# Performance work log

Hardware: AMD Instinct MI355X
Metric: run time of the kernel (lower is better)

The kernel has to match this reference:

```python
import jax, jax.numpy as jnp
import numpy as np
import math

NLAT, NLON = 46, 90      # equiangular grid (in_shape == out_shape)
CH = 256                 # channels == kdim == vdim
BATCH = 1

def _cc_weights(n):
    # Clenshaw-Curtis quadrature weights (Waldvogel), nodes cos(k*pi/(n-1)); matches torch-harmonics equiangular grid
    n1 = n - 1
    N = np.arange(1, n1, 2)
    l = len(N)
    m = n1 - l
    v = np.concatenate([2.0 / N / (N - 2), [1.0 / N[-1]], np.zeros(m)])
    v = -v[:-1] - v[-1:0:-1]
    g0 = -np.ones(n1)
    g0[l] += n1
    g0[m] += n1
    g = g0 / (n1 ** 2 - 1 + (n1 % 2))
    w = np.fft.ifft(v + g).real
    return np.concatenate([w, w[:1]])

def _precompute_sparsity():
    # replicates _precompute_neighborhood_sparsity_s2: YZY-rotated north pole indicator within theta_cutoff
    lats = np.linspace(0.0, math.pi, NLAT)               # colatitudes of equiangular grid
    quad = (2.0 * math.pi / NLON) * _cc_weights(NLAT)    # per-latitude quadrature weights
    cutoff = math.pi / (NLAT - 1)                        # default theta_cutoff
    lons = np.linspace(0.0, 2.0 * math.pi, NLON + 1)[:-1]
    rows, cols = [], []
    for t in range(NLAT):
        a = -lats[t]
        beta = lons[None, :]
        gamma = lats[:, None]
        z = -np.cos(beta) * np.sin(a) * np.sin(gamma) + np.cos(a) * np.cos(gamma)
        x = np.cos(a) * np.cos(beta) * np.sin(gamma) + np.cos(gamma) * np.sin(a)
        y = np.sin(beta) * np.sin(gamma)
        nrm = np.sqrt(x * x + y * y + z * z)
        theta = np.arccos(np.clip(z / nrm, -1.0, 1.0))
        ii, jj = np.nonzero(theta <= cutoff)
        rows.append(np.full(ii.shape, t, dtype=np.int64))
        cols.append(ii * NLON + jj)
    row_ids = np.concatenate(rows).astype(np.int32)   # CSR row id per nnz (sorted)
    col_idx = np.concatenate(cols).astype(np.int32)   # flattened input index (at wo=0)
    return row_ids, col_idx, quad.astype(np.float32)

def setup_inputs() -> dict:
    key = jax.random.key(0)
    ks = jax.random.split(key, 9)
    row_ids, col_idx, quad = _precompute_sparsity()
    scale = 0.02  # sane init scale (module uses raw randn; trained weights would be O(this))
    return {
        "qo": jax.random.normal(ks[0], (BATCH, CH, NLAT, NLON), dtype=jnp.float32),
        "ki": jax.random.normal(ks[1], (BATCH, CH, NLAT, NLON), dtype=jnp.float32),
        "vi": jax.random.normal(ks[2], (BATCH, CH, NLAT, NLON), dtype=jnp.float32),
        "q_w": jax.random.normal(ks[3], (CH, CH), dtype=jnp.float32) * scale,
        "k_w": jax.random.normal(ks[4], (CH, CH), dtype=jnp.float32) * scale,
        "v_w": jax.random.normal(ks[5], (CH, CH), dtype=jnp.float32) * scale,
        "q_b": jax.random.normal(ks[6], (CH,), dtype=jnp.float32) * scale,
        "k_b": jax.random.normal(ks[7], (CH,), dtype=jnp.float32) * scale,
        "v_b": jax.random.normal(ks[8], (CH,), dtype=jnp.float32) * scale,
        "quad_w": jnp.asarray(quad),
        "row_ids": jnp.asarray(row_ids),
        "col_idx": jnp.asarray(col_idx),
    }

def reference(qo, ki, vi, q_w, k_w, v_w, q_b, k_b, v_b, quad_w, row_ids, col_idx):
    nlat, nlon = qo.shape[2], qo.shape[3]
    # 1x1 conv projections (F.conv2d with [out,in,1,1] kernels)
    q = jnp.einsum("kc,bchw->bkhw", q_w, qo) + q_b[None, :, None, None]
    k = jnp.einsum("kc,bchw->bkhw", k_w, ki) + k_b[None, :, None, None]
    v = jnp.einsum("vc,bchw->bvhw", v_w, vi) + v_b[None, :, None, None]

    hi = col_idx // nlon                                   # [N] input latitude per nnz
    wi0 = col_idx % nlon                                   # [N] input longitude at wo=0
    wo = jnp.arange(nlon)
    wi = (wi0[:, None] + wo[None, :]) % nlon               # [N, nlon] longitudes rotated by output lon

    kg = k[:, :, hi[:, None], wi]                          # [B, kdim, N, nlon] gathered keys
    qg = q[:, :, row_ids, :]                               # [B, kdim, N, nlon] query of owning output row
    qdotk = jnp.einsum("bcnw,bcnw->nbw", qg, kg)           # [N, B, nlon]

    # quadrature-weighted softmax over each output point's neighborhood (segment = output latitude row)
    seg_max = jax.ops.segment_max(qdotk, row_ids, num_segments=nlat, indices_are_sorted=True)
    seg_max = jax.lax.stop_gradient(seg_max)               # max shift cancels exactly in the ratio
    alpha = jnp.exp(qdotk - seg_max[row_ids]) * quad_w[hi][:, None, None]   # [N, B, nlon]
    denom = jax.ops.segment_sum(alpha, row_ids, num_segments=nlat, indices_are_sorted=True)  # [nlat, B, nlon]

    vg = jnp.transpose(v[:, :, hi[:, None], wi], (2, 0, 1, 3))   # [N, B, vdim, nlon]
    num = jax.ops.segment_sum(alpha[:, :, None, :] * vg, row_ids, num_segments=nlat, indices_are_sorted=True)
    out = num / denom[:, :, None, :]                       # [nlat, B, vdim, nlon]
    return jnp.transpose(out, (1, 2, 0, 3))                # [B, vdim, nlat, nlon]
```

## Files before the change

### kernel.cpp

```cpp
#include <hip/hip_runtime.h>
#include <math.h>

#define NLAT 46
#define NLON 90
#define CH   256
#define HW   (NLAT*NLON)
#define HWP  4160

#define LIGHT_PER_XCD 473
#define SLOTS_PER_XCD (45 + LIGHT_PER_XCD)

typedef __attribute__((ext_vector_type(8))) short short8;
typedef __attribute__((ext_vector_type(4))) float floatx4;

__device__ __forceinline__ ushort f2bf(float f){
  uint u = __float_as_uint(f);
  u += 0x7fff + ((u >> 16) & 1);
  return (ushort)(u >> 16);
}
__device__ __forceinline__ float bf2f(ushort u){
  return __uint_as_float(((uint)u) << 16);
}

__device__ __forceinline__ int lower_bound_i(const int* __restrict__ a, int n, int key){
  int lo = 0, hi = n;
  while (lo < hi){ int mid = (lo + hi) >> 1; if (a[mid] < key) lo = mid + 1; else hi = mid; }
  return lo;
}

__global__ __launch_bounds__(256) void cast_w_kernel(
    const float* __restrict__ qw, const float* __restrict__ kw, const float* __restrict__ vw,
    ushort* __restrict__ Wq, ushort* __restrict__ Wk, ushort* __restrict__ Wv)
{
  const float* W; ushort* O;
  if (blockIdx.x == 0){ W = qw; O = Wq; }
  else if (blockIdx.x == 1){ W = kw; O = Wk; }
  else { W = vw; O = Wv; }
  for (int i = threadIdx.x; i < (CH*CH)/4; i += 256){
    float4 w = ((const float4*)W)[i];
    ushort4 o;
    o.x = f2bf(w.x); o.y = f2bf(w.y); o.z = f2bf(w.z); o.w = f2bf(w.w);
    ((ushort4*)O)[i] = o;
  }
}

__global__ __launch_bounds__(256) void transpose_cast_kernel(
    const float* __restrict__ qo, const float* __restrict__ ki, const float* __restrict__ vi,
    ushort* __restrict__ qX, ushort* __restrict__ kX, ushort* __restrict__ vX)
{
  const float* X; ushort* O;
  if (blockIdx.z == 0){ X = qo; O = qX; }
  else if (blockIdx.z == 1){ X = ki; O = kX; }
  else { X = vi; O = vX; }

  __shared__ float T[64][65];

  const int tid = threadIdx.x;
  const int hw0 = blockIdx.x * 64;
  const int c0  = blockIdx.y * 64;

  {
    int hwL = tid & 63;
    int cb  = tid >> 6;
    int hw  = hw0 + hwL;
    #pragma unroll
    for (int it = 0; it < 16; it++){
      int cL = cb + it*4;
      T[cL][hwL] = (hw < HW) ? X[(size_t)(c0+cL)*HW + hw] : 0.f;
    }
  }
  __syncthreads();
  {
    int cpair = tid & 31;
    int rb    = tid >> 5;
    #pragma unroll
    for (int it = 0; it < 8; it++){
      int r = rb + it*8;
      float v0 = T[2*cpair][r];
      float v1 = T[2*cpair+1][r];
      ushort2 o; o.x = f2bf(v0); o.y = f2bf(v1);
      *(ushort2*)(O + (size_t)(hw0 + r)*CH + c0 + 2*cpair) = o;
    }
  }
}

__global__ __launch_bounds__(256) void proj_kernel(
    const ushort* __restrict__ qX, const ushort* __restrict__ kX, const ushort* __restrict__ vX,
    const ushort* __restrict__ Wq, const ushort* __restrict__ Wk, const ushort* __restrict__ Wv,
    const float* __restrict__ qb, const float* __restrict__ kb, const float* __restrict__ vb,
    ushort* __restrict__ qP, ushort* __restrict__ kP, ushort* __restrict__ vP)
{
  const ushort *Xt, *Wb; const float* Bias; ushort* Out;
  if (blockIdx.z == 0){ Xt = qX; Wb = Wq; Bias = qb; Out = qP; }
  else if (blockIdx.z == 1){ Xt = kX; Wb = Wk; Bias = kb; Out = kP; }
  else { Xt = vX; Wb = Wv; Bias = vb; Out = vP; }

  const int tid  = threadIdx.x;
  const int lane = tid & 63;
  const int wave = tid >> 6;
  const int hw_w   = blockIdx.x * 64 + (wave >> 1) * 32;
  const int kout_w = blockIdx.y * 64 + (wave & 1) * 32;

  const int lm = lane & 15;
  const int lq = lane >> 4;

  const ushort* a0p = Wb + (size_t)(kout_w + lm)*CH + lq*8;
  const ushort* a1p = a0p + 16*CH;
  const ushort* b0p = Xt + (size_t)(hw_w + lm)*CH + lq*8;
  const ushort* b1p = b0p + 16*CH;

  floatx4 acc00 = {0,0,0,0}, acc01 = {0,0,0,0}, acc10 = {0,0,0,0}, acc11 = {0,0,0,0};

  #pragma unroll
  for (int k0 = 0; k0 < 8; k0++){
    int off = k0 * 32;
    short8 a0 = *(const short8*)(a0p + off);
    short8 a1 = *(const short8*)(a1p + off);
    short8 b0 = *(const short8*)(b0p + off);
    short8 b1 = *(const short8*)(b1p + off);
    acc00 = __builtin_amdgcn_mfma_f32_16x16x32_bf16(a0, b0, acc00, 0, 0, 0);
    acc01 = __builtin_amdgcn_mfma_f32_16x16x32_bf16(a0, b1, acc01, 0, 0, 0);
    acc10 = __builtin_amdgcn_mfma_f32_16x16x32_bf16(a1, b0, acc10, 0, 0, 0);
    acc11 = __builtin_amdgcn_mfma_f32_16x16x32_bf16(a1, b1, acc11, 0, 0, 0);
  }

  #pragma unroll
  for (int i = 0; i < 2; i++){
    int kout = kout_w + i*16 + lq*4;
    float4 bias = *(const float4*)(Bias + kout);
    #pragma unroll
    for (int j = 0; j < 2; j++){
      floatx4 c;
      if (i == 0) c = (j == 0) ? acc00 : acc01;
      else        c = (j == 0) ? acc10 : acc11;
      int hw = hw_w + j*16 + lm;
      if (hw < HW){
        ushort4 o;
        o.x = f2bf(c[0] + bias.x);
        o.y = f2bf(c[1] + bias.y);
        o.z = f2bf(c[2] + bias.z);
        o.w = f2bf(c[3] + bias.w);
        *(ushort4*)(Out + (size_t)hw*CH + kout) = o;
      }
    }
  }
}

__device__ __forceinline__ float4 ld_bf4(const ushort* p, int lane){
  ushort4 u = ((const ushort4*)p)[lane];
  float4 f;
  f.x = bf2f(u.x); f.y = bf2f(u.y); f.z = bf2f(u.z); f.w = bf2f(u.w);
  return f;
}

__global__ __launch_bounds__(256) void attn_kernel(
    const ushort* __restrict__ qP, const ushort* __restrict__ kP, const ushort* __restrict__ vP,
    const float* __restrict__ quad_w, const int* __restrict__ row_ids,
    const int* __restrict__ col_idx, int nnz, float* __restrict__ out)
{
  const int bid  = blockIdx.x;
  const int xcd  = bid & 7;
  const int slot = bid >> 3;

  int t, wo;
  if (slot < 45){
    int hu   = xcd * 45 + slot;
    int hidx = hu / 90;
    t  = (hidx < 2) ? hidx : 42 + hidx;
    wo = hu - hidx * 90;
  } else {
    int lu = xcd * LIGHT_PER_XCD + (slot - 45);
    if (lu >= 42 * NLON) return;
    int li = lu / NLON;
    t  = li + 2;
    wo = lu - li * NLON;
  }

  const int tid  = threadIdx.x;
  const int lane = tid & 63;
  const int wave = tid >> 6;

  const int start = lower_bound_i(row_ids, nnz, t);
  const int end   = lower_bound_i(row_ids, nnz, t + 1);

  const float4 qf = ld_bf4(qP + (size_t)(t * NLON + wo) * CH, lane);

  float denom = 0.f;
  float4 acc = make_float4(0.f, 0.f, 0.f, 0.f);

  int n = start + wave;
  for (; n + 4 < end; n += 8){
    int ciA = col_idx[n];
    int hiA = ciA / NLON;
    int wiA = ciA - hiA*NLON + wo; if (wiA >= NLON) wiA -= NLON;
    size_t offA = ((size_t)hiA*NLON + wiA) * CH;
    int ciB = col_idx[n + 4];
    int hiB = ciB / NLON;
    int wiB = ciB - hiB*NLON + wo; if (wiB >= NLON) wiB -= NLON;
    size_t offB = ((size_t)hiB*NLON + wiB) * CH;

    float4 kfA = ld_bf4(kP + offA, lane);
    float4 kfB = ld_bf4(kP + offB, lane);
    float sA = qf.x*kfA.x + qf.y*kfA.y + qf.z*kfA.z + qf.w*kfA.w;
    float sB = qf.x*kfB.x + qf.y*kfB.y + qf.z*kfB.z + qf.w*kfB.w;
    #pragma unroll
    for (int o = 32; o >= 1; o >>= 1){
      sA += __shfl_xor(sA, o, 64);
      sB += __shfl_xor(sB, o, 64);
    }
    float eA = __expf(sA) * quad_w[hiA];
    float eB = __expf(sB) * quad_w[hiB];
    float4 vfA = ld_bf4(vP + offA, lane);
    float4 vfB = ld_bf4(vP + offB, lane);
    denom += eA + eB;
    acc.x += eA*vfA.x + eB*vfB.x;
    acc.y += eA*vfA.y + eB*vfB.y;
    acc.z += eA*vfA.z + eB*vfB.z;
    acc.w += eA*vfA.w + eB*vfB.w;
  }
  if (n < end){
    int ci = col_idx[n];
    int hi = ci / NLON;
    int wi = ci - hi*NLON + wo; if (wi >= NLON) wi -= NLON;
    size_t off = ((size_t)hi*NLON + wi) * CH;
    float4 kf = ld_bf4(kP + off, lane);
    float s = qf.x*kf.x + qf.y*kf.y + qf.z*kf.z + qf.w*kf.w;
    #pragma unroll
    for (int o = 32; o >= 1; o >>= 1) s += __shfl_xor(s, o, 64);
    float e = __expf(s) * quad_w[hi];
    float4 vf = ld_bf4(vP + off, lane);
    denom += e;
    acc.x += e*vf.x; acc.y += e*vf.y; acc.z += e*vf.z; acc.w += e*vf.w;
  }

  __shared__ float sden[4];
  __shared__ float sacc[4][CH];
  if (lane == 0) sden[wave] = denom;
  sacc[wave][lane*4+0] = acc.x;
  sacc[wave][lane*4+1] = acc.y;
  sacc[wave][lane*4+2] = acc.z;
  sacc[wave][lane*4+3] = acc.w;
  __syncthreads();

  const float den = sden[0] + sden[1] + sden[2] + sden[3];
  const float num = sacc[0][tid] + sacc[1][tid] + sacc[2][tid] + sacc[3][tid];
  out[(size_t)tid * HW + t * NLON + wo] = num / den;
}

extern "C" void kernel_launch(void* const* d_in, const int* in_sizes, int n_in,
                              void* d_out, int out_size, void* d_ws, size_t ws_size,
                              hipStream_t stream)
{
  const float* qo   = (const float*)d_in[0];
  const float* ki   = (const float*)d_in[1];
  const float* vi   = (const float*)d_in[2];
  const float* qw   = (const float*)d_in[3];
  const float* kw   = (const float*)d_in[4];
  const float* vw   = (const float*)d_in[5];
  const float* qb   = (const float*)d_in[6];
  const float* kb   = (const float*)d_in[7];
  const float* vb   = (const float*)d_in[8];
  const float* quad = (const float*)d_in[9];
  const int* row_ids = (const int*)d_in[10];
  const int* col_idx = (const int*)d_in[11];
  const int nnz = in_sizes[10];

  ushort* ws = (ushort*)d_ws;
  const size_t TSZ = (size_t)HWP * CH;
  ushort* qX = ws;              ushort* kX = qX + TSZ;  ushort* vX = kX + TSZ;
  ushort* qP = vX + TSZ;        ushort* kP = qP + TSZ;  ushort* vP = kP + TSZ;
  ushort* Wq = vP + TSZ;        ushort* Wk = Wq + CH*CH; ushort* Wv = Wk + CH*CH;

  cast_w_kernel<<<dim3(3), 256, 0, stream>>>(qw, kw, vw, Wq, Wk, Wv);
  transpose_cast_kernel<<<dim3(65, 4, 3), 256, 0, stream>>>(qo, ki, vi, qX, kX, vX);
  proj_kernel<<<dim3(65, 4, 3), 256, 0, stream>>>(qX, kX, vX, Wq, Wk, Wv, qb, kb, vb, qP, kP, vP);
  attn_kernel<<<dim3(8 * SLOTS_PER_XCD), 256, 0, stream>>>(qP, kP, vP, quad, row_ids, col_idx, nnz, (float*)d_out);
}
```

Before: 141.9 us.

## Fuse transpose-cast into projection GEMM via shared-memory staging

The separate transpose/cast kernel and the bf16 intermediate round trip through global memory are replaced by a fused projection kernel. Each block loads a 32-position tile of fp32 input across all channels, converts it to bf16 in LDS, and each wave computes a 64-output-channel slice with MFMA. The weight-cast kernel is also spread over 8 blocks per matrix instead of one. This removes a kernel launch and an intermediate write and read, at the cost of strided fp32 loads and fewer, larger projection blocks.

```diff
diff --git a/kernel.cpp b/kernel.cpp
--- a/kernel.cpp
+++ b/kernel.cpp
@@ -6,6 +6,9 @@
 #define CH   256
 #define HW   (NLAT*NLON)
 #define HWP  4160
+#define HWT  32
+#define NHT  130
+#define XSTR 264
 
 #define LIGHT_PER_XCD 473
 #define SLOTS_PER_XCD (45 + LIGHT_PER_XCD)
@@ -33,10 +36,10 @@
     ushort* __restrict__ Wq, ushort* __restrict__ Wk, ushort* __restrict__ Wv)
 {
   const float* W; ushort* O;
-  if (blockIdx.x == 0){ W = qw; O = Wq; }
-  else if (blockIdx.x == 1){ W = kw; O = Wk; }
+  if (blockIdx.y == 0){ W = qw; O = Wq; }
+  else if (blockIdx.y == 1){ W = kw; O = Wk; }
   else { W = vw; O = Wv; }
-  for (int i = threadIdx.x; i < (CH*CH)/4; i += 256){
+  for (int i = blockIdx.x * 256 + threadIdx.x; i < (CH*CH)/4; i += 8*256){
     float4 w = ((const float4*)W)[i];
     ushort4 o;
     o.x = f2bf(w.x); o.y = f2bf(w.y); o.z = f2bf(w.z); o.w = f2bf(w.w);
@@ -44,102 +47,84 @@
   }
 }
 
-__global__ __launch_bounds__(256) void transpose_cast_kernel(
+__global__ __launch_bounds__(256) void fproj_kernel(
     const float* __restrict__ qo, const float* __restrict__ ki, const float* __restrict__ vi,
-    ushort* __restrict__ qX, ushort* __restrict__ kX, ushort* __restrict__ vX)
-{
-  const float* X; ushort* O;
-  if (blockIdx.z == 0){ X = qo; O = qX; }
-  else if (blockIdx.z == 1){ X = ki; O = kX; }
-  else { X = vi; O = vX; }
-
-  __shared__ float T[64][65];
-
-  const int tid = threadIdx.x;
-  const int hw0 = blockIdx.x * 64;
-  const int c0  = blockIdx.y * 64;
-
-  {
-    int hwL = tid & 63;
-    int cb  = tid >> 6;
-    int hw  = hw0 + hwL;
-    #pragma unroll
-    for (int it = 0; it < 16; it++){
-      int cL = cb + it*4;
-      T[cL][hwL] = (hw < HW) ? X[(size_t)(c0+cL)*HW + hw] : 0.f;
-    }
-  }
-  __syncthreads();
-  {
-    int cpair = tid & 31;
-    int rb    = tid >> 5;
-    #pragma unroll
-    for (int it = 0; it < 8; it++){
-      int r = rb + it*8;
-      float v0 = T[2*cpair][r];
-      float v1 = T[2*cpair+1][r];
-      ushort2 o; o.x = f2bf(v0); o.y = f2bf(v1);
-      *(ushort2*)(O + (size_t)(hw0 + r)*CH + c0 + 2*cpair) = o;
-    }
-  }
-}
-
-__global__ __launch_bounds__(256) void proj_kernel(
-    const ushort* __restrict__ qX, const ushort* __restrict__ kX, const ushort* __restrict__ vX,
     const ushort* __restrict__ Wq, const ushort* __restrict__ Wk, const ushort* __restrict__ Wv,
     const float* __restrict__ qb, const float* __restrict__ kb, const float* __restrict__ vb,
     ushort* __restrict__ qP, ushort* __restrict__ kP, ushort* __restrict__ vP)
 {
-  const ushort *Xt, *Wb; const float* Bias; ushort* Out;
-  if (blockIdx.z == 0){ Xt = qX; Wb = Wq; Bias = qb; Out = qP; }
-  else if (blockIdx.z == 1){ Xt = kX; Wb = Wk; Bias = kb; Out = kP; }
-  else { Xt = vX; Wb = Wv; Bias = vb; Out = vP; }
-
-  const int tid  = threadIdx.x;
+  const float* X; const ushort* Wb; const float* Bias; ushort* Out;
+  if (blockIdx.y == 0){ X = qo; Wb = Wq; Bias = qb; Out = qP; }
+  else if (blockIdx.y == 1){ X = ki; Wb = Wk; Bias = kb; Out = kP; }
+  else { X = vi; Wb = Wv; Bias = vb; Out = vP; }
+
+  __shared__ ushort Xs[HWT][XSTR];
+
+  const int tid = threadIdx.x;
+  const int hw0 = blockIdx.x * HWT;
+
+  {
+    int hwL = tid & 31;
+    int cb  = tid >> 5;
+    int hw  = hw0 + hwL;
+    bool ok = hw < HW;
+    const float* Xp = X + (size_t)(cb*32)*HW + (ok ? hw : 0);
+    #pragma unroll
+    for (int g = 0; g < 4; g++){
+      short8 pk;
+      #pragma unroll
+      for (int u = 0; u < 8; u++){
+        float f = ok ? Xp[(size_t)(g*8 + u)*HW] : 0.f;
+        pk[u] = (short)f2bf(f);
+      }
+      *(short8*)(&Xs[hwL][cb*32 + g*8]) = pk;
+    }
+  }
+  __syncthreads();
+
   const int lane = tid & 63;
   const int wave = tid >> 6;
-  const int hw_w   = blockIdx.x * 64 + (wave >> 1) * 32;
-  const int kout_w = blockIdx.y * 64 + (wave & 1) * 32;
-
   const int lm = lane & 15;
   const int lq = lane >> 4;
-
-  const ushort* a0p = Wb + (size_t)(kout_w + lm)*CH + lq*8;
-  const ushort* a1p = a0p + 16*CH;
-  const ushort* b0p = Xt + (size_t)(hw_w + lm)*CH + lq*8;
-  const ushort* b1p = b0p + 16*CH;
-
-  floatx4 acc00 = {0,0,0,0}, acc01 = {0,0,0,0}, acc10 = {0,0,0,0}, acc11 = {0,0,0,0};
+  const int kout_w = wave * 64;
+
+  const ushort* Ap = Wb + (size_t)(kout_w + lm)*CH + lq*8;
+
+  floatx4 acc[4][2];
+  #pragma unroll
+  for (int i = 0; i < 4; i++)
+    #pragma unroll
+    for (int j = 0; j < 2; j++) acc[i][j] = (floatx4){0,0,0,0};
 
   #pragma unroll
   for (int k0 = 0; k0 < 8; k0++){
-    int off = k0 * 32;
-    short8 a0 = *(const short8*)(a0p + off);
-    short8 a1 = *(const short8*)(a1p + off);
-    short8 b0 = *(const short8*)(b0p + off);
-    short8 b1 = *(const short8*)(b1p + off);
-    acc00 = __builtin_amdgcn_mfma_f32_16x16x32_bf16(a0, b0, acc00, 0, 0, 0);
-    acc01 = __builtin_amdgcn_mfma_f32_16x16x32_bf16(a0, b1, acc01, 0, 0, 0);
-    acc10 = __builtin_amdgcn_mfma_f32_16x16x32_bf16(a1, b0, acc10, 0, 0, 0);
-    acc11 = __builtin_amdgcn_mfma_f32_16x16x32_bf16(a1, b1, acc11, 0, 0, 0);
+    short8 a[4], b[2];
+    #pragma unroll
+    for (int i = 0; i < 4; i++)
+      a[i] = *(const short8*)(Ap + (size_t)i*16*CH + k0*32);
+    #pragma unroll
+    for (int j = 0; j < 2; j++)
+      b[j] = *(const short8*)(&Xs[j*16 + lm][lq*8 + k0*32]);
+    #pragma unroll
+    for (int i = 0; i < 4; i++)
+      #pragma unroll
+      for (int j = 0; j < 2; j++)
+        acc[i][j] = __builtin_amdgcn_mfma_f32_16x16x32_bf16(a[i], b[j], acc[i][j], 0, 0, 0);
   }
 
   #pragma unroll
-  for (int i = 0; i < 2; i++){
+  for (int i = 0; i < 4; i++){
     int kout = kout_w + i*16 + lq*4;
     float4 bias = *(const float4*)(Bias + kout);
     #pragma unroll
     for (int j = 0; j < 2; j++){
-      floatx4 c;
-      if (i == 0) c = (j == 0) ? acc00 : acc01;
-      else        c = (j == 0) ? acc10 : acc11;
-      int hw = hw_w + j*16 + lm;
+      int hw = hw0 + j*16 + lm;
       if (hw < HW){
         ushort4 o;
-        o.x = f2bf(c[0] + bias.x);
-        o.y = f2bf(c[1] + bias.y);
-        o.z = f2bf(c[2] + bias.z);
-        o.w = f2bf(c[3] + bias.w);
+        o.x = f2bf(acc[i][j][0] + bias.x);
+        o.y = f2bf(acc[i][j][1] + bias.y);
+        o.z = f2bf(acc[i][j][2] + bias.z);
+        o.w = f2bf(acc[i][j][3] + bias.w);
         *(ushort4*)(Out + (size_t)hw*CH + kout) = o;
       }
     }
@@ -267,12 +252,10 @@
 
   ushort* ws = (ushort*)d_ws;
   const size_t TSZ = (size_t)HWP * CH;
-  ushort* qX = ws;              ushort* kX = qX + TSZ;  ushort* vX = kX + TSZ;
-  ushort* qP = vX + TSZ;        ushort* kP = qP + TSZ;  ushort* vP = kP + TSZ;
-  ushort* Wq = vP + TSZ;        ushort* Wk = Wq + CH*CH; ushort* Wv = Wk + CH*CH;
-
-  cast_w_kernel<<<dim3(3), 256, 0, stream>>>(qw, kw, vw, Wq, Wk, Wv);
-  transpose_cast_kernel<<<dim3(65, 4, 3), 256, 0, stream>>>(qo, ki, vi, qX, kX, vX);
-  proj_kernel<<<dim3(65, 4, 3), 256, 0, stream>>>(qX, kX, vX, Wq, Wk, Wv, qb, kb, vb, qP, kP, vP);
+  ushort* qP = ws;        ushort* kP = qP + TSZ;   ushort* vP = kP + TSZ;
+  ushort* Wq = vP + TSZ;  ushort* Wk = Wq + CH*CH; ushort* Wv = Wk + CH*CH;
+
+  cast_w_kernel<<<dim3(8, 3), 256, 0, stream>>>(qw, kw, vw, Wq, Wk, Wv);
+  fproj_kernel<<<dim3(NHT, 3), 256, 0, stream>>>(qo, ki, vi, Wq, Wk, Wv, qb, kb, vb, qP, kP, vP);
   attn_kernel<<<dim3(8 * SLOTS_PER_XCD), 256, 0, stream>>>(qP, kP, vP, quad, row_ids, col_idx, nnz, (float*)d_out);
 }
```

Result: faster. 124.1 us (-12.5%).
